# Optimization experiments

Measured on AMD Instinct MI355X. Metric: run time of the kernel, lower is better.

Reference implementation:

```python
import jax, jax.numpy as jnp
import numpy as np

N, TI, TO1 = 8, 200, 51
V, E, H, J, L = 1024, 512, 512, 512, 3
ENC_D = 512


def setup_inputs() -> dict:
    key = jax.random.key(0)
    ks = jax.random.split(key, 11)
    s = lambda k, shape, sc: jax.random.normal(k, shape, jnp.float32) * sc
    return {
        "enc_out": s(ks[0], (N, TI, ENC_D), 1.0),
        "tgt_pad": jax.random.randint(ks[1], (N, TO1), 0, V),
        "embed": s(ks[2], (V, E), 0.02),          # nn.Embedding weight
        "w_ih": s(ks[3], (L, 4 * H, E), 0.04),    # LSTM input-hidden (gate order i,f,g,o)
        "w_hh": s(ks[4], (L, 4 * H, H), 0.04),    # LSTM hidden-hidden
        "b_ih": s(ks[5], (L, 4 * H), 0.04),
        "b_hh": s(ks[6], (L, 4 * H), 0.04),
        "enc_w": s(ks[7], (J, ENC_D), 0.04),      # enc_proj (no bias)
        "dec_w": s(ks[8], (J, H), 0.04),          # dec_proj weight
        "dec_b": s(ks[9], (J,), 0.04),            # dec_proj bias
        "out_w": s(ks[10], (V, J), 0.04),         # output (no bias)
    }


def lstm_layer(x, wih, whh, bih, bhh):
    # x: [N, T, E] -> [N, T, H]; PyTorch LSTM gate order i, f, g, o
    n = x.shape[0]
    h0 = jnp.zeros((n, whh.shape[1]), x.dtype)
    c0 = jnp.zeros_like(h0)
    gin = jnp.einsum('nte,ge->ntg', x, wih) + bih + bhh  # precompute input contributions

    def step(carry, g_t):
        h, c = carry
        g = g_t + h @ whh.T
        i, f, gg, o = jnp.split(g, 4, axis=-1)
        c = jax.nn.sigmoid(f) * c + jax.nn.sigmoid(i) * jnp.tanh(gg)
        h = jax.nn.sigmoid(o) * jnp.tanh(c)
        return (h, c), h

    _, hs = jax.lax.scan(step, (h0, c0), jnp.swapaxes(gin, 0, 1))
    return jnp.swapaxes(hs, 0, 1)


def reference(enc_out, tgt_pad, embed, w_ih, w_hh, b_ih, b_hh, enc_w, dec_w, dec_b, out_w):
    # embedding lookup
    x = embed[tgt_pad]                                   # [N, To+1, E]
    # 3-layer unidirectional LSTM
    for l in range(w_ih.shape[0]):
        x = lstm_layer(x, w_ih[l], w_hh[l], b_ih[l], b_hh[l])
    # projections
    enc_p = jnp.einsum('ntd,jd->ntj', enc_out, enc_w)    # [N, Ti, J]
    dec_p = jnp.einsum('nud,jd->nuj', x, dec_w) + dec_b  # [N, To+1, J]
    # joint: broadcast add -> tanh -> output linear (no bias)
    add = enc_p[:, :, None, :] + dec_p[:, None, :, :]    # [N, Ti, To+1, J]
    return jnp.einsum('ntuj,vj->ntuv', jnp.tanh(add), out_w)  # [N, Ti, To+1, V]
```

## Files before the change

kernel.cpp:

```cpp
#include <hip/hip_runtime.h>
#include <cstdint>
#include <cstddef>

typedef __attribute__((ext_vector_type(4))) float f32x4;
typedef __attribute__((ext_vector_type(8))) short bf16x8;
typedef __attribute__((ext_vector_type(8))) unsigned short u16x8;
typedef __attribute__((ext_vector_type(4))) float float4v;
typedef __attribute__((ext_vector_type(2))) unsigned long long u64x2;
typedef unsigned long long ull;

#define NB   8
#define TIN  200
#define TO1  51
#define VSZ  1024
#define HSZ  512
static constexpr int MJOINT = NB * TIN * TO1;
static constexpr int MROWS  = TO1 * NB;

static constexpr size_t B_ENCBF = 0;
static constexpr size_t B_ENCW  = B_ENCBF + 1664ull*512*2;
static constexpr size_t B_DECW  = B_ENCW  + 512ull*512*2;
static constexpr size_t B_OUTW  = B_DECW  + 512ull*512*2;
static constexpr size_t B_WIH   = B_OUTW  + 1024ull*512*2;
static constexpr size_t B_WHH   = B_WIH   + 3ull*2048*512*2;
static constexpr size_t B_XTR   = B_WHH   + 3ull*2048*512*2;
static constexpr size_t B_BSUM  = B_XTR   + 4ull*408*512*2;
static constexpr size_t B_FLAGS = B_BSUM  + 3ull*2048*4;
static constexpr size_t B_ENCP  = B_FLAGS + 8192;
static constexpr size_t B_DECP  = B_ENCP  + 1664ull*512*4;
static constexpr size_t B_ABUF  = B_DECP  + 512ull*512*4;

__device__ __forceinline__ unsigned short f2bf(float f) {
  union { float f; unsigned u; } v; v.f = f;
  unsigned r = v.u + 0x7FFFu + ((v.u >> 16) & 1u);
  return (unsigned short)(r >> 16);
}
__device__ __forceinline__ float fast_tanh(float x) {
  float t = __expf(2.0f * x);
  return 1.0f - 2.0f / (t + 1.0f);
}
__device__ __forceinline__ float fast_sig(float x) {
  return 1.0f / (1.0f + __expf(-x));
}
__device__ __forceinline__ void gll16(const void* g, void* l) {
  __builtin_amdgcn_global_load_lds(
      (const __attribute__((address_space(1))) unsigned int*)g,
      (__attribute__((address_space(3))) unsigned int*)l, 16, 0, 0);
}
__device__ __forceinline__ void cvt8(const float* s, unsigned short* d) {
  const float4v* sp = (const float4v*)s;
  float4v x = sp[0], y = sp[1];
  u16x8 o;
  o[0]=f2bf(x[0]); o[1]=f2bf(x[1]); o[2]=f2bf(x[2]); o[3]=f2bf(x[3]);
  o[4]=f2bf(y[0]); o[5]=f2bf(y[1]); o[6]=f2bf(y[2]); o[7]=f2bf(y[3]);
  *(u16x8*)d = o;
}

static constexpr int N_ENC  = 102400;
static constexpr int N_ENCW = 32768;
static constexpr int N_DECW = 32768;
static constexpr int N_OUTW = 65536;
static constexpr int N_WIH  = 393216;
static constexpr int P0 = N_ENC, P1 = P0+N_ENCW, P2 = P1+N_DECW, P3 = P2+N_OUTW,
                     P4 = P3+N_WIH;

__global__ __launch_bounds__(256) void prep_all(const float* __restrict__ enc,
                                                const float* __restrict__ encw,
                                                const float* __restrict__ decw,
                                                const float* __restrict__ outw,
                                                const float* __restrict__ wih,
                                                const float* __restrict__ whh,
                                                const float* __restrict__ emb,
                                                const int* __restrict__ tgt,
                                                const float* __restrict__ bih,
                                                const float* __restrict__ bhh,
                                                unsigned short* __restrict__ d_enc,
                                                unsigned short* __restrict__ d_encw,
                                                unsigned short* __restrict__ d_decw,
                                                unsigned short* __restrict__ d_outw,
                                                unsigned short* __restrict__ d_wih,
                                                unsigned short* __restrict__ d_whh,
                                                unsigned short* __restrict__ x0,
                                                float* __restrict__ bsum,
                                                int* __restrict__ flags) {
  if (blockIdx.x == 0 && threadIdx.x < 96) flags[threadIdx.x * 16] = 0;
  if (blockIdx.x >= 4086) {
    int i = (blockIdx.x - 4086) * 2048 + threadIdx.x * 8;
#pragma unroll
    for (int k = 0; k < 8; ++k) bsum[i + k] = bih[i + k] + bhh[i + k];
    return;
  }
  if (blockIdx.x >= 3984) {
    int idx = (blockIdx.x - 3984) * 256 + threadIdx.x;
    if (idx >= MROWS * 64) return;
    int m = idx >> 6, kc = (idx & 63) * 8;
    int t = m >> 3, n = m & 7;
    int v = tgt[n * TO1 + t];
    cvt8(emb + (size_t)v * 512 + kc, x0 + (size_t)m * 512 + kc);
    return;
  }
  int i = blockIdx.x * 256 + threadIdx.x;
  const float* s; unsigned short* d; int rel;
  if      (i < P0) { s = enc;  d = d_enc;  rel = i; }
  else if (i < P1) { s = encw; d = d_encw; rel = i - P0; }
  else if (i < P2) { s = decw; d = d_decw; rel = i - P1; }
  else if (i < P3) { s = outw; d = d_outw; rel = i - P2; }
  else if (i < P4) { s = wih;  d = d_wih;  rel = i - P3; }
  else             { s = whh;  d = d_whh;  rel = i - P4; }
  cvt8(s + (size_t)rel * 8, d + (size_t)rel * 8);
}

__global__ __launch_bounds__(256) void gemm_bf16(const unsigned short* __restrict__ A,
                                                 const unsigned short* __restrict__ B,
                                                 float* __restrict__ C,
                                                 const float* __restrict__ bias,
                                                 int M, int N, int K) {
  __shared__ __align__(16) unsigned short lds[2][2][4096];
  const int tid = threadIdx.x;
  const int wave = tid >> 6, lane = tid & 63;
  const int lr = lane & 15, lg = lane >> 4;
  const int wm = (wave >> 1) * 64, wn = (wave & 1) * 64;
  const int xsl = (lg ^ (lr & 3)) << 3;

  const int nwg = gridDim.x * gridDim.y;
  const int id = blockIdx.y * gridDim.x + blockIdx.x;
  const int q = nwg >> 3, r = nwg & 7, xcd = id & 7, rest = id >> 3;
  const int nid = (xcd < r ? xcd * (q + 1) : r * (q + 1) + (xcd - r) * q) + rest;
  const size_t n0 = (size_t)(nid % gridDim.x) * 128;
  const size_t m0 = (size_t)(nid / gridDim.x) * 128;

  f32x4 acc[4][4];
#pragma unroll
  for (int i = 0; i < 4; ++i)
#pragma unroll
    for (int j = 0; j < 4; ++j) acc[i][j] = (f32x4){0.f, 0.f, 0.f, 0.f};

#define STAGE(bf, kt)                                                                 \
  do {                                                                                \
    _Pragma("unroll") for (int u = 0; u < 2; ++u) {                                   \
      const int s = u * 256 + tid;                                                    \
      const int row_ = s >> 2;                                                        \
      const int ch = (s & 3) ^ (row_ & 3);                                            \
      gll16(A + (m0 + row_) * (size_t)K + (kt) + ch * 8,                              \
            &lds[bf][0][(u * 256 + wave * 64) * 8]);                                  \
    }                                                                                 \
    _Pragma("unroll") for (int u = 0; u < 2; ++u) {                                   \
      const int s = u * 256 + tid;                                                    \
      const int row_ = s >> 2;                                                        \
      const int ch = (s & 3) ^ (row_ & 3);                                            \
      gll16(B + (n0 + row_) * (size_t)K + (kt) + ch * 8,                              \
            &lds[bf][1][(u * 256 + wave * 64) * 8]);                                  \
    }                                                                                 \
  } while (0)

  const int nt = K >> 5;
  int cur = 0;
  STAGE(0, 0);
  for (int t = 0; t < nt; ++t) {
    if (t + 1 < nt) {
      STAGE(cur ^ 1, (t + 1) * 32);
      asm volatile("s_waitcnt vmcnt(4)" ::: "memory");
    } else {
      asm volatile("s_waitcnt vmcnt(0)" ::: "memory");
    }
    __builtin_amdgcn_s_barrier();
    const unsigned short* As_ = lds[cur][0];
    const unsigned short* Bs_ = lds[cur][1];
    bf16x8 a[4], b[4];
#pragma unroll
    for (int i = 0; i < 4; ++i) a[i] = *(const bf16x8*)&As_[(wm + i * 16 + lr) * 32 + xsl];
#pragma unroll
    for (int j = 0; j < 4; ++j) b[j] = *(const bf16x8*)&Bs_[(wn + j * 16 + lr) * 32 + xsl];
    __builtin_amdgcn_s_setprio(1);
#pragma unroll
    for (int i = 0; i < 4; ++i)
#pragma unroll
      for (int j = 0; j < 4; ++j)
        acc[i][j] = __builtin_amdgcn_mfma_f32_16x16x32_bf16(a[i], b[j], acc[i][j], 0, 0, 0);
    __builtin_amdgcn_s_setprio(0);
    __builtin_amdgcn_s_barrier();
    cur ^= 1;
  }
#undef STAGE

  const int rq = lg * 4;
#pragma unroll
  for (int j = 0; j < 4; ++j) {
    const int col = (int)n0 + wn + j * 16 + lr;
    const float bv = bias ? bias[col] : 0.0f;
#pragma unroll
    for (int i = 0; i < 4; ++i) {
#pragma unroll
      for (int q2 = 0; q2 < 4; ++q2) {
        const long m = (long)m0 + wm + i * 16 + rq + q2;
        if (m < M) C[(size_t)m * N + col] = acc[i][j][q2] + bv;
      }
    }
  }
}

__global__ __launch_bounds__(512, 2) void gemm256(const unsigned short* __restrict__ A,
                                                  const unsigned short* __restrict__ B,
                                                  float* __restrict__ C,
                                                  int M, int N, int K) {
  __shared__ __align__(16) unsigned short lds[2][2][8192];
  const int tid = threadIdx.x;
  const int wave = tid >> 6, lane = tid & 63;
  const int lr = lane & 15, lg = lane >> 4;
  const int wr = (wave >> 2) * 128;
  const int wc = (wave & 3) * 64;

  const int nwg = gridDim.x * gridDim.y;
  const int id = blockIdx.y * gridDim.x + blockIdx.x;
  const int q = nwg >> 3, r = nwg & 7, xcd = id & 7, rest = id >> 3;
  const int nid = (xcd < r ? xcd * (q + 1) : r * (q + 1) + (xcd - r) * q) + rest;
  const size_t n0 = (size_t)(nid % gridDim.x) * 256;
  const size_t m0 = (size_t)(nid / gridDim.x) * 256;

  f32x4 acc[8][4];
#pragma unroll
  for (int i = 0; i < 8; ++i)
#pragma unroll
    for (int j = 0; j < 4; ++j) acc[i][j] = (f32x4){0.f, 0.f, 0.f, 0.f};

#define STG(bf, kt)                                                                    \
  do {                                                                                 \
    _Pragma("unroll") for (int u = 0; u < 2; ++u) {                                    \
      const int idx = u * 512 + tid;                                                   \
      const int row_ = idx >> 2;                                                       \
      const int ch = (idx & 3) ^ (row_ & 3);                                           \
      gll16(A + (m0 + row_) * (size_t)K + (kt) + ch * 8,                               \
            &lds[bf][0][(u * 512 + wave * 64) * 8]);                                   \
    }                                                                                  \
    _Pragma("unroll") for (int u = 0; u < 2; ++u) {                                    \
      const int idx = u * 512 + tid;                                                   \
      const int row_ = idx >> 2;                                                       \
      const int ch = (idx & 3) ^ (row_ & 3);                                           \
      gll16(B + (n0 + row_) * (size_t)K + (kt) + ch * 8,                               \
            &lds[bf][1][(u * 512 + wave * 64) * 8]);                                   \
    }                                                                                  \
  } while (0)

  const int nt = K >> 5;
  int cur = 0;
  STG(0, 0);
  for (int t = 0; t < nt; ++t) {
    if (t + 1 < nt) {
      STG(cur ^ 1, (t + 1) * 32);
      asm volatile("s_waitcnt vmcnt(4)" ::: "memory");
    } else {
      asm volatile("s_waitcnt vmcnt(0)" ::: "memory");
    }
    __builtin_amdgcn_s_barrier();
    const unsigned short* As_ = lds[cur][0];
    const unsigned short* Bs_ = lds[cur][1];
    bf16x8 b[4];
#pragma unroll
    for (int j = 0; j < 4; ++j) {
      const int rb = wc + j * 16 + lr;
      b[j] = *(const bf16x8*)&Bs_[rb * 32 + ((lg ^ (rb & 3)) << 3)];
    }
    __builtin_amdgcn_s_setprio(1);
#pragma unroll
    for (int i = 0; i < 8; ++i) {
      const int ra = wr + i * 16 + lr;
      bf16x8 a0 = *(const bf16x8*)&As_[ra * 32 + ((lg ^ (ra & 3)) << 3)];
#pragma unroll
      for (int j = 0; j < 4; ++j)
        acc[i][j] = __builtin_amdgcn_mfma_f32_16x16x32_bf16(a0, b[j], acc[i][j], 0, 0, 0);
    }
    __builtin_amdgcn_s_setprio(0);
    __builtin_amdgcn_s_barrier();
    cur ^= 1;
  }
#undef STG

#pragma unroll
  for (int i = 0; i < 8; ++i) {
#pragma unroll
    for (int q2 = 0; q2 < 4; ++q2) {
      const long m = (long)m0 + wr + i * 16 + lg * 4 + q2;
      if (m < M) {
        float* crow = C + (size_t)m * N + n0 + wc;
#pragma unroll
        for (int j = 0; j < 4; ++j) crow[j * 16 + lr] = acc[i][j][q2];
      }
    }
  }
}

__global__ __launch_bounds__(256) void tanha_kernel(const float* __restrict__ encp,
                                                    const float* __restrict__ decp,
                                                    unsigned short* __restrict__ Ab) {
  size_t idx = (size_t)blockIdx.x * 256 + threadIdx.x;
  int m = (int)(idx >> 6);
  int kc = ((int)idx & 63) * 8;
  if (m >= 81664) return;
  u16x8 o;
  if (m >= MJOINT) {
    o[0]=0;o[1]=0;o[2]=0;o[3]=0;o[4]=0;o[5]=0;o[6]=0;o[7]=0;
  } else {
    int n = m / (TIN * TO1);
    int rem = m - n * (TIN * TO1);
    int t = rem / TO1;
    int u = rem - t * TO1;
    const float4v* ep = (const float4v*)(encp + ((size_t)n * TIN + t) * 512 + kc);
    const float4v* dp = (const float4v*)(decp + ((size_t)u * 8 + n) * 512 + kc);
    float4v e0 = ep[0], e1 = ep[1], d0 = dp[0], d1 = dp[1];
    o[0]=f2bf(fast_tanh(e0[0]+d0[0])); o[1]=f2bf(fast_tanh(e0[1]+d0[1]));
    o[2]=f2bf(fast_tanh(e0[2]+d0[2])); o[3]=f2bf(fast_tanh(e0[3]+d0[3]));
    o[4]=f2bf(fast_tanh(e1[0]+d1[0])); o[5]=f2bf(fast_tanh(e1[1]+d1[1]));
    o[6]=f2bf(fast_tanh(e1[2]+d1[2])); o[7]=f2bf(fast_tanh(e1[3]+d1[3]));
  }
  *(u16x8*)(Ab + (size_t)m * 512 + kc) = o;
}

__global__ __launch_bounds__(256) void rnn_enc_kernel(const unsigned short* __restrict__ wih,
                                                      const unsigned short* __restrict__ whh,
                                                      const float* __restrict__ bsum,
                                                      unsigned short* __restrict__ xtr,
                                                      int* __restrict__ flags,
                                                      const unsigned short* __restrict__ eA,
                                                      const unsigned short* __restrict__ eB,
                                                      float* __restrict__ eC) {
  __shared__ __align__(16) unsigned short w_s[64 * 1024];
  __shared__ __align__(16) unsigned short x_s[8 * 512];
  __shared__ __align__(16) unsigned short h_s[8 * 512];
  __shared__ float gates_s[4][8][16];

  const int tid = threadIdx.x;
  const int wave = tid >> 6, lane = tid & 63;
  const int lr = lane & 15, lg = lane >> 4;

  if (blockIdx.x >= 96) {
    unsigned short* eld = w_s;
    const int g = blockIdx.x - 96;
    const int wm = (wave >> 1) * 64, wn = (wave & 1) * 64;
    const int xsl = (lg ^ (lr & 3)) << 3;
    const int nwg = 52;
    const int q = nwg >> 3, r = nwg & 7, xcd = g & 7, rest = g >> 3;
    const int nid = (xcd < r ? xcd * (q + 1) : r * (q + 1) + (xcd - r) * q) + rest;
    const size_t n0 = (size_t)(nid & 3) * 128;
    const size_t m0 = (size_t)(nid >> 2) * 128;

    f32x4 acc[4][4];
#pragma unroll
    for (int i = 0; i < 4; ++i)
#pragma unroll
      for (int j = 0; j < 4; ++j) acc[i][j] = (f32x4){0.f, 0.f, 0.f, 0.f};

#define ESTG(bf, kt)                                                                   \
    do {                                                                               \
      _Pragma("unroll") for (int u = 0; u < 2; ++u) {                                  \
        const int s = u * 256 + tid;                                                   \
        const int row_ = s >> 2;                                                       \
        const int ch = (s & 3) ^ (row_ & 3);                                           \
        gll16(eA + (m0 + row_) * 512 + (kt) + ch * 8,                                  \
              &eld[(bf) * 8192 + (u * 256 + wave * 64) * 8]);                          \
      }                                                                                \
      _Pragma("unroll") for (int u = 0; u < 2; ++u) {                                  \
        const int s = u * 256 + tid;                                                   \
        const int row_ = s >> 2;                                                       \
        const int ch = (s & 3) ^ (row_ & 3);                                           \
        gll16(eB + (n0 + row_) * 512 + (kt) + ch * 8,                                  \
              &eld[(bf) * 8192 + 4096 + (u * 256 + wave * 64) * 8]);                   \
      }                                                                                \
    } while (0)

    int cur = 0;
    ESTG(0, 0);
    for (int t = 0; t < 16; ++t) {
      if (t + 1 < 16) {
        ESTG(cur ^ 1, (t + 1) * 32);
        asm volatile("s_waitcnt vmcnt(4)" ::: "memory");
      } else {
        asm volatile("s_waitcnt vmcnt(0)" ::: "memory");
      }
      __builtin_amdgcn_s_barrier();
      const unsigned short* As_ = eld + cur * 8192;
      const unsigned short* Bs_ = As_ + 4096;
      bf16x8 a[4], b[4];
#pragma unroll
      for (int i = 0; i < 4; ++i) a[i] = *(const bf16x8*)&As_[(wm + i * 16 + lr) * 32 + xsl];
#pragma unroll
      for (int j = 0; j < 4; ++j) b[j] = *(const bf16x8*)&Bs_[(wn + j * 16 + lr) * 32 + xsl];
      __builtin_amdgcn_s_setprio(1);
#pragma unroll
      for (int i = 0; i < 4; ++i)
#pragma unroll
        for (int j = 0; j < 4; ++j)
          acc[i][j] = __builtin_amdgcn_mfma_f32_16x16x32_bf16(a[i], b[j], acc[i][j], 0, 0, 0);
      __builtin_amdgcn_s_setprio(0);
      __builtin_amdgcn_s_barrier();
      cur ^= 1;
    }
#undef ESTG

    const int rq = lg * 4;
#pragma unroll
    for (int j = 0; j < 4; ++j) {
      const int col = (int)n0 + wn + j * 16 + lr;
#pragma unroll
      for (int i = 0; i < 4; ++i) {
#pragma unroll
        for (int q2 = 0; q2 < 4; ++q2) {
          const long m = (long)m0 + wm + i * 16 + rq + q2;
          eC[(size_t)m * 512 + col] = acc[i][j][q2];
        }
      }
    }
    return;
  }

  const int l = blockIdx.x >> 5;
  const int b32 = blockIdx.x & 31;
  const int hid0 = b32 << 4;
  const int r7 = lr & 7;
  const int rw = wave * 16 + lr;

  {
    const int rl = tid >> 2;
    const int qt = tid & 3;
    const size_t R = (size_t)l * 2048 + (size_t)(rl >> 4) * 512 + hid0 + (rl & 15);
    const unsigned short* s0 = wih + R * 512;
    const unsigned short* s1 = whh + R * 512;
#pragma unroll
    for (int i = 0; i < 32; ++i) {
      int c = qt * 32 + i;
      bf16x8 wv = (c < 64) ? *(const bf16x8*)&s0[c * 8] : *(const bf16x8*)&s1[(c - 64) * 8];
      *(bf16x8*)&w_s[rl * 1024 + ((c ^ (rl & 7)) << 3)] = wv;
    }
  }
  const float bias = bsum[(size_t)l * 2048 + (size_t)wave * 512 + hid0 + lr];

  const unsigned short* xin = xtr + (size_t)l * MROWS * 512;
  unsigned short* xout = xtr + (size_t)(l + 1) * MROWS * 512;
  float c_reg = 0.f;
  const int srow = tid >> 5;
  const int sc = tid & 31;
  __syncthreads();

#define ALOAD(P) __hip_atomic_load((P), __ATOMIC_RELAXED, __HIP_MEMORY_SCOPE_AGENT)

  f32x4 ax0, ax1;

  if (l > 0) {
    if (wave == 0) {
      for (;;) {
        bool ok_ = true;
        if (lane < 32)
          ok_ = ALOAD(&flags[((l - 1) * 32 + lane) * 16]) >= 1;
        if (__all(ok_)) break;
        __builtin_amdgcn_s_sleep(1);
      }
    }
  }
  __syncthreads();
  {
    const ull* px = (const ull*)(xin + (size_t)srow * 512);
#pragma unroll
    for (int k_ = 0; k_ < 2; ++k_) {
      const int c_ = sc + k_ * 32;
      ull v0 = ALOAD(px + c_ * 2), v1 = ALOAD(px + c_ * 2 + 1);
      *(u64x2*)&x_s[srow * 512 + ((c_ ^ srow) << 3)] = (u64x2){v0, v1};
    }
  }
  __syncthreads();
  ax0 = (f32x4){0.f, 0.f, 0.f, 0.f};
  ax1 = (f32x4){0.f, 0.f, 0.f, 0.f};
#pragma unroll
  for (int c16 = 0; c16 < 16; ++c16) {
    const int cc = c16 * 4 + lg;
    bf16x8 av = *(const bf16x8*)&x_s[r7 * 512 + ((cc ^ r7) << 3)];
    bf16x8 bv = *(const bf16x8*)&w_s[rw * 1024 + ((cc ^ r7) << 3)];
    if (c16 & 1) ax1 = __builtin_amdgcn_mfma_f32_16x16x32_bf16(av, bv, ax1, 0, 0, 0);
    else         ax0 = __builtin_amdgcn_mfma_f32_16x16x32_bf16(av, bv, ax0, 0, 0, 0);
  }

  for (int t = 0; t < TO1; ++t) {
    const bool doH = (t > 0);
    const bool doX = (t + 1 < TO1);
    if (doH || (doX && l > 0)) {
      if (wave == 0) {
        for (;;) {
          bool ok_ = true;
          if (lane < 32) {
            if (doH) ok_ = ALOAD(&flags[(l * 32 + lane) * 16]) >= t;
          } else {
            if (doX && l > 0)
              ok_ = ALOAD(&flags[((l - 1) * 32 + (lane - 32)) * 16]) >= t + 2;
          }
          if (__all(ok_)) break;
          __builtin_amdgcn_s_sleep(1);
        }
      }
    }
    __syncthreads();

    {
      ull vh[4], vx[4];
      const ull* ph = (const ull*)(xout + ((size_t)(t - 1) * 8 + srow) * 512);
      const ull* px = (const ull*)(xin + ((size_t)(t + 1) * 8 + srow) * 512);
#pragma unroll
      for (int k_ = 0; k_ < 2; ++k_) {
        const int c_ = sc + k_ * 32;
        if (doH) { vh[2 * k_] = ALOAD(ph + c_ * 2); vh[2 * k_ + 1] = ALOAD(ph + c_ * 2 + 1); }
        if (doX) { vx[2 * k_] = ALOAD(px + c_ * 2); vx[2 * k_ + 1] = ALOAD(px + c_ * 2 + 1); }
      }
#pragma unroll
      for (int k_ = 0; k_ < 2; ++k_) {
        const int c_ = sc + k_ * 32;
        if (doH) *(u64x2*)&h_s[srow * 512 + ((c_ ^ srow) << 3)] = (u64x2){vh[2 * k_], vh[2 * k_ + 1]};
        if (doX) *(u64x2*)&x_s[srow * 512 + ((c_ ^ srow) << 3)] = (u64x2){vx[2 * k_], vx[2 * k_ + 1]};
      }
    }
    __syncthreads();

    f32x4 acc0 = ax0, acc1 = ax1;
    if (doH) {
#pragma unroll
      for (int c16 = 0; c16 < 16; ++c16) {
        const int cc = c16 * 4 + lg;
        bf16x8 av = *(const bf16x8*)&h_s[r7 * 512 + ((cc ^ r7) << 3)];
        bf16x8 bv = *(const bf16x8*)&w_s[rw * 1024 + (((64 + cc) ^ r7) << 3)];
        if (c16 & 1) acc1 = __builtin_amdgcn_mfma_f32_16x16x32_bf16(av, bv, acc1, 0, 0, 0);
        else         acc0 = __builtin_amdgcn_mfma_f32_16x16x32_bf16(av, bv, acc0, 0, 0, 0);
      }
    }

    {
      f32x4 g = acc0 + acc1;
      const int nb4 = lg * 4;
#pragma unroll
      for (int q2 = 0; q2 < 4; ++q2) {
        int n = nb4 + q2;
        if (n < 8) gates_s[wave][n][lr] = g[q2] + bias;
      }
    }
    __syncthreads();
    if (tid < 128) {
      const int n = tid >> 4, j = tid & 15;
      float gi = gates_s[0][n][j], gf = gates_s[1][n][j];
      float gg = gates_s[2][n][j], go = gates_s[3][n][j];
      c_reg = fast_sig(gf) * c_reg + fast_sig(gi) * fast_tanh(gg);
      float ht = fast_sig(go) * fast_tanh(c_reg);
      float htn = __shfl_down(ht, 1);
      if (!(j & 1)) {
        unsigned pk = (unsigned)f2bf(ht) | ((unsigned)f2bf(htn) << 16);
        unsigned* dst = (unsigned*)(xout + ((size_t)t * 8 + n) * 512 + hid0 + j);
        __hip_atomic_store(dst, pk, __ATOMIC_RELAXED, __HIP_MEMORY_SCOPE_AGENT);
      }
    }
    asm volatile("s_waitcnt vmcnt(0)" ::: "memory");
    __syncthreads();
    if (tid == 0)
      __hip_atomic_store(&flags[(l * 32 + b32) * 16], t + 1,
                         __ATOMIC_RELAXED, __HIP_MEMORY_SCOPE_AGENT);

    if (doX) {
      ax0 = (f32x4){0.f, 0.f, 0.f, 0.f};
      ax1 = (f32x4){0.f, 0.f, 0.f, 0.f};
#pragma unroll
      for (int c16 = 0; c16 < 16; ++c16) {
        const int cc = c16 * 4 + lg;
        bf16x8 av = *(const bf16x8*)&x_s[r7 * 512 + ((cc ^ r7) << 3)];
        bf16x8 bv = *(const bf16x8*)&w_s[rw * 1024 + ((cc ^ r7) << 3)];
        if (c16 & 1) ax1 = __builtin_amdgcn_mfma_f32_16x16x32_bf16(av, bv, ax1, 0, 0, 0);
        else         ax0 = __builtin_amdgcn_mfma_f32_16x16x32_bf16(av, bv, ax0, 0, 0, 0);
      }
    }
  }
#undef ALOAD
}

extern "C" void kernel_launch(void* const* d_in, const int* in_sizes, int n_in,
                              void* d_out, int out_size, void* d_ws, size_t ws_size,
                              hipStream_t stream) {
  (void)in_sizes; (void)n_in; (void)out_size; (void)ws_size;
  const float* enc_out = (const float*)d_in[0];
  const int*   tgt     = (const int*)d_in[1];
  const float* embed   = (const float*)d_in[2];
  const float* w_ih    = (const float*)d_in[3];
  const float* w_hh    = (const float*)d_in[4];
  const float* b_ih    = (const float*)d_in[5];
  const float* b_hh    = (const float*)d_in[6];
  const float* enc_w   = (const float*)d_in[7];
  const float* dec_w   = (const float*)d_in[8];
  const float* dec_b   = (const float*)d_in[9];
  const float* out_w   = (const float*)d_in[10];

  char* ws = (char*)d_ws;
  unsigned short* enc_bf  = (unsigned short*)(ws + B_ENCBF);
  unsigned short* encw_bf = (unsigned short*)(ws + B_ENCW);
  unsigned short* decw_bf = (unsigned short*)(ws + B_DECW);
  unsigned short* outw_bf = (unsigned short*)(ws + B_OUTW);
  unsigned short* wih_bf  = (unsigned short*)(ws + B_WIH);
  unsigned short* whh_bf  = (unsigned short*)(ws + B_WHH);
  unsigned short* xtr     = (unsigned short*)(ws + B_XTR);
  float* bsum  = (float*)(ws + B_BSUM);
  int*   flags = (int*)(ws + B_FLAGS);
  float* encp  = (float*)(ws + B_ENCP);
  float* decp  = (float*)(ws + B_DECP);
  unsigned short* abuf = (unsigned short*)(ws + B_ABUF);
  float* Cout  = (float*)d_out;

  prep_all<<<4089, 256, 0, stream>>>(enc_out, enc_w, dec_w, out_w, w_ih, w_hh,
                                     embed, tgt, b_ih, b_hh,
                                     enc_bf, encw_bf, decw_bf, outw_bf, wih_bf, whh_bf,
                                     xtr, bsum, flags);

  rnn_enc_kernel<<<148, 256, 0, stream>>>(wih_bf, whh_bf, bsum, xtr, flags,
                                          enc_bf, encw_bf, encp);

  gemm_bf16<<<dim3(4, 4), 256, 0, stream>>>(xtr + 3ull * MROWS * 512, decw_bf, decp, dec_b,
                                            MROWS, 512, 512);
  tanha_kernel<<<20416, 256, 0, stream>>>(encp, decp, abuf);
  gemm256<<<dim3(4, 319), 512, 0, stream>>>(abuf, outw_bf, Cout, MJOINT, VSZ, 512);
}
```

Measured before the change: 347.7 us.

## Fuse decoder projection and tanh-join into persistent RNN kernel with flag-driven workers

Removes the separate dec_proj GEMM and tanh/add kernels. 102 extra workgroups are added to the persistent RNN/encoder kernel. Each one polls the layer-3 timestep flags and a new encoder-projection completion counter, then computes its dec_p row with MFMA and writes the tanh(enc_p+dec_p) bf16 activations. The aim is to hide joint-input preparation behind the serial LSTM recurrence and save two launches. The risks are that the bandwidth-heavy tanh stage now runs on only 102 workgroups, the last timestep's work stays exposed at the tail, all workgroups must be co-resident, and the padding rows of abuf are no longer zeroed.

New measurement: 336.4 us. -3.2%, faster.

```diff
diff --git a/kernel.cpp b/kernel.cpp
--- a/kernel.cpp
+++ b/kernel.cpp
@@ -55,6 +55,8 @@
   o[4]=f2bf(y[0]); o[5]=f2bf(y[1]); o[6]=f2bf(y[2]); o[7]=f2bf(y[3]);
   *(u16x8*)d = o;
 }
+#define ALOAD(P)     __hip_atomic_load((P), __ATOMIC_RELAXED, __HIP_MEMORY_SCOPE_AGENT)
+#define ASTORE(P, V) __hip_atomic_store((P), (V), __ATOMIC_RELAXED, __HIP_MEMORY_SCOPE_AGENT)
 
 static constexpr int N_ENC  = 102400;
 static constexpr int N_ENCW = 32768;
@@ -83,7 +85,7 @@
                                                 unsigned short* __restrict__ x0,
                                                 float* __restrict__ bsum,
                                                 int* __restrict__ flags) {
-  if (blockIdx.x == 0 && threadIdx.x < 96) flags[threadIdx.x * 16] = 0;
+  if (blockIdx.x == 0 && threadIdx.x < 97) flags[threadIdx.x * 16] = 0;
   if (blockIdx.x >= 4086) {
     int i = (blockIdx.x - 4086) * 2048 + threadIdx.x * 8;
 #pragma unroll
@@ -108,95 +110,6 @@
   else if (i < P4) { s = wih;  d = d_wih;  rel = i - P3; }
   else             { s = whh;  d = d_whh;  rel = i - P4; }
   cvt8(s + (size_t)rel * 8, d + (size_t)rel * 8);
-}
-
-__global__ __launch_bounds__(256) void gemm_bf16(const unsigned short* __restrict__ A,
-                                                 const unsigned short* __restrict__ B,
-                                                 float* __restrict__ C,
-                                                 const float* __restrict__ bias,
-                                                 int M, int N, int K) {
-  __shared__ __align__(16) unsigned short lds[2][2][4096];
-  const int tid = threadIdx.x;
-  const int wave = tid >> 6, lane = tid & 63;
-  const int lr = lane & 15, lg = lane >> 4;
-  const int wm = (wave >> 1) * 64, wn = (wave & 1) * 64;
-  const int xsl = (lg ^ (lr & 3)) << 3;
-
-  const int nwg = gridDim.x * gridDim.y;
-  const int id = blockIdx.y * gridDim.x + blockIdx.x;
-  const int q = nwg >> 3, r = nwg & 7, xcd = id & 7, rest = id >> 3;
-  const int nid = (xcd < r ? xcd * (q + 1) : r * (q + 1) + (xcd - r) * q) + rest;
-  const size_t n0 = (size_t)(nid % gridDim.x) * 128;
-  const size_t m0 = (size_t)(nid / gridDim.x) * 128;
-
-  f32x4 acc[4][4];
-#pragma unroll
-  for (int i = 0; i < 4; ++i)
-#pragma unroll
-    for (int j = 0; j < 4; ++j) acc[i][j] = (f32x4){0.f, 0.f, 0.f, 0.f};
-
-#define STAGE(bf, kt)                                                                 \
-  do {                                                                                \
-    _Pragma("unroll") for (int u = 0; u < 2; ++u) {                                   \
-      const int s = u * 256 + tid;                                                    \
-      const int row_ = s >> 2;                                                        \
-      const int ch = (s & 3) ^ (row_ & 3);                                            \
-      gll16(A + (m0 + row_) * (size_t)K + (kt) + ch * 8,                              \
-            &lds[bf][0][(u * 256 + wave * 64) * 8]);                                  \
-    }                                                                                 \
-    _Pragma("unroll") for (int u = 0; u < 2; ++u) {                                   \
-      const int s = u * 256 + tid;                                                    \
-      const int row_ = s >> 2;                                                        \
-      const int ch = (s & 3) ^ (row_ & 3);                                            \
-      gll16(B + (n0 + row_) * (size_t)K + (kt) + ch * 8,                              \
-            &lds[bf][1][(u * 256 + wave * 64) * 8]);                                  \
-    }                                                                                 \
-  } while (0)
-
-  const int nt = K >> 5;
-  int cur = 0;
-  STAGE(0, 0);
-  for (int t = 0; t < nt; ++t) {
-    if (t + 1 < nt) {
-      STAGE(cur ^ 1, (t + 1) * 32);
-      asm volatile("s_waitcnt vmcnt(4)" ::: "memory");
-    } else {
-      asm volatile("s_waitcnt vmcnt(0)" ::: "memory");
-    }
-    __builtin_amdgcn_s_barrier();
-    const unsigned short* As_ = lds[cur][0];
-    const unsigned short* Bs_ = lds[cur][1];
-    bf16x8 a[4], b[4];
-#pragma unroll
-    for (int i = 0; i < 4; ++i) a[i] = *(const bf16x8*)&As_[(wm + i * 16 + lr) * 32 + xsl];
-#pragma unroll
-    for (int j = 0; j < 4; ++j) b[j] = *(const bf16x8*)&Bs_[(wn + j * 16 + lr) * 32 + xsl];
-    __builtin_amdgcn_s_setprio(1);
-#pragma unroll
-    for (int i = 0; i < 4; ++i)
-#pragma unroll
-      for (int j = 0; j < 4; ++j)
-        acc[i][j] = __builtin_amdgcn_mfma_f32_16x16x32_bf16(a[i], b[j], acc[i][j], 0, 0, 0);
-    __builtin_amdgcn_s_setprio(0);
-    __builtin_amdgcn_s_barrier();
-    cur ^= 1;
-  }
-#undef STAGE
-
-  const int rq = lg * 4;
-#pragma unroll
-  for (int j = 0; j < 4; ++j) {
-    const int col = (int)n0 + wn + j * 16 + lr;
-    const float bv = bias ? bias[col] : 0.0f;
-#pragma unroll
-    for (int i = 0; i < 4; ++i) {
-#pragma unroll
-      for (int q2 = 0; q2 < 4; ++q2) {
-        const long m = (long)m0 + wm + i * 16 + rq + q2;
-        if (m < M) C[(size_t)m * N + col] = acc[i][j][q2] + bv;
-      }
-    }
-  }
 }
 
 __global__ __launch_bounds__(512, 2) void gemm256(const unsigned short* __restrict__ A,
@@ -289,40 +202,18 @@
   }
 }
 
-__global__ __launch_bounds__(256) void tanha_kernel(const float* __restrict__ encp,
-                                                    const float* __restrict__ decp,
-                                                    unsigned short* __restrict__ Ab) {
-  size_t idx = (size_t)blockIdx.x * 256 + threadIdx.x;
-  int m = (int)(idx >> 6);
-  int kc = ((int)idx & 63) * 8;
-  if (m >= 81664) return;
-  u16x8 o;
-  if (m >= MJOINT) {
-    o[0]=0;o[1]=0;o[2]=0;o[3]=0;o[4]=0;o[5]=0;o[6]=0;o[7]=0;
-  } else {
-    int n = m / (TIN * TO1);
-    int rem = m - n * (TIN * TO1);
-    int t = rem / TO1;
-    int u = rem - t * TO1;
-    const float4v* ep = (const float4v*)(encp + ((size_t)n * TIN + t) * 512 + kc);
-    const float4v* dp = (const float4v*)(decp + ((size_t)u * 8 + n) * 512 + kc);
-    float4v e0 = ep[0], e1 = ep[1], d0 = dp[0], d1 = dp[1];
-    o[0]=f2bf(fast_tanh(e0[0]+d0[0])); o[1]=f2bf(fast_tanh(e0[1]+d0[1]));
-    o[2]=f2bf(fast_tanh(e0[2]+d0[2])); o[3]=f2bf(fast_tanh(e0[3]+d0[3]));
-    o[4]=f2bf(fast_tanh(e1[0]+d1[0])); o[5]=f2bf(fast_tanh(e1[1]+d1[1]));
-    o[6]=f2bf(fast_tanh(e1[2]+d1[2])); o[7]=f2bf(fast_tanh(e1[3]+d1[3]));
-  }
-  *(u16x8*)(Ab + (size_t)m * 512 + kc) = o;
-}
-
-__global__ __launch_bounds__(256) void rnn_enc_kernel(const unsigned short* __restrict__ wih,
-                                                      const unsigned short* __restrict__ whh,
-                                                      const float* __restrict__ bsum,
-                                                      unsigned short* __restrict__ xtr,
-                                                      int* __restrict__ flags,
-                                                      const unsigned short* __restrict__ eA,
-                                                      const unsigned short* __restrict__ eB,
-                                                      float* __restrict__ eC) {
+__global__ __launch_bounds__(256) void mega_kernel(const unsigned short* __restrict__ wih,
+                                                   const unsigned short* __restrict__ whh,
+                                                   const float* __restrict__ bsum,
+                                                   unsigned short* __restrict__ xtr,
+                                                   int* __restrict__ flags,
+                                                   const unsigned short* __restrict__ eA,
+                                                   const unsigned short* __restrict__ eB,
+                                                   float* __restrict__ eC,
+                                                   const unsigned short* __restrict__ decw,
+                                                   const float* __restrict__ dec_b,
+                                                   const float* __restrict__ encp,
+                                                   unsigned short* __restrict__ abuf) {
   __shared__ __align__(16) unsigned short w_s[64 * 1024];
   __shared__ __align__(16) unsigned short x_s[8 * 512];
   __shared__ __align__(16) unsigned short h_s[8 * 512];
@@ -331,6 +222,81 @@
   const int tid = threadIdx.x;
   const int wave = tid >> 6, lane = tid & 63;
   const int lr = lane & 15, lg = lane >> 4;
+  const int r7 = lr & 7;
+
+  if (blockIdx.x >= 148) {
+    const int wkr = blockIdx.x - 148;
+    unsigned short* h3_s = x_s;
+    float* decp_row = (float*)w_s;
+    const unsigned short* xtr3 = xtr + 3ull * MROWS * 512;
+#pragma unroll 1
+    for (int k = 0; k < 4; ++k) {
+      const int j = wkr + 102 * k;
+      const int u = j >> 3;
+      const int p = j & 7;
+      if (wave == 0) {
+        for (;;) {
+          bool ok = true;
+          if (lane < 32) ok = ALOAD(&flags[(64 + lane) * 16]) >= u + 1;
+          else if (lane == 32) ok = ALOAD(&flags[96 * 16]) >= 52;
+          if (__all(ok)) break;
+          __builtin_amdgcn_s_sleep(1);
+        }
+      }
+      __syncthreads();
+      {
+        const int sr2 = tid >> 5, sc2 = tid & 31;
+        const ull* ph = (const ull*)(xtr3 + ((size_t)u * 8 + sr2) * 512);
+#pragma unroll
+        for (int k2 = 0; k2 < 2; ++k2) {
+          const int c_ = sc2 + k2 * 32;
+          ull v0 = ALOAD(ph + c_ * 2), v1 = ALOAD(ph + c_ * 2 + 1);
+          *(u64x2*)&h3_s[sr2 * 512 + ((c_ ^ sr2) << 3)] = (u64x2){v0, v1};
+        }
+      }
+      __syncthreads();
+      {
+        const int colbase = wave * 128;
+#pragma unroll
+        for (int ct = 0; ct < 8; ++ct) {
+          f32x4 acc = (f32x4){0.f, 0.f, 0.f, 0.f};
+          const int col = colbase + ct * 16 + lr;
+#pragma unroll
+          for (int c16 = 0; c16 < 16; ++c16) {
+            const int cc = c16 * 4 + lg;
+            bf16x8 av = *(const bf16x8*)&h3_s[r7 * 512 + ((cc ^ r7) << 3)];
+            bf16x8 bv = *(const bf16x8*)&decw[(size_t)col * 512 + cc * 8];
+            acc = __builtin_amdgcn_mfma_f32_16x16x32_bf16(av, bv, acc, 0, 0, 0);
+          }
+#pragma unroll
+          for (int q2 = 0; q2 < 4; ++q2)
+            if (lg * 4 + q2 == p) decp_row[col] = acc[q2] + dec_b[col];
+        }
+      }
+      __syncthreads();
+      {
+        const int tr = tid >> 6;
+        const int colc = (lane) * 8;
+        for (int pass = 0; pass < 50; ++pass) {
+          const int nt = p * 200 + pass * 4 + tr;
+          const ull* pe = (const ull*)(encp + (size_t)nt * 512 + colc);
+          ull ev[4];
+#pragma unroll
+          for (int k2 = 0; k2 < 4; ++k2) ev[k2] = ALOAD(pe + k2);
+          float ef[8];
+          *(u64x2*)&ef[0] = (u64x2){ev[0], ev[1]};
+          *(u64x2*)&ef[4] = (u64x2){ev[2], ev[3]};
+          u16x8 o;
+#pragma unroll
+          for (int w2 = 0; w2 < 8; ++w2)
+            o[w2] = f2bf(fast_tanh(ef[w2] + decp_row[colc + w2]));
+          *(u16x8*)&abuf[((size_t)nt * TO1 + u) * 512 + colc] = o;
+        }
+      }
+      __syncthreads();
+    }
+    return;
+  }
 
   if (blockIdx.x >= 96) {
     unsigned short* eld = w_s;
@@ -405,17 +371,20 @@
 #pragma unroll
         for (int q2 = 0; q2 < 4; ++q2) {
           const long m = (long)m0 + wm + i * 16 + rq + q2;
-          eC[(size_t)m * 512 + col] = acc[i][j][q2];
+          ASTORE(&eC[(size_t)m * 512 + col], acc[i][j][q2]);
         }
       }
     }
+    asm volatile("s_waitcnt vmcnt(0)" ::: "memory");
+    __syncthreads();
+    if (tid == 0)
+      __hip_atomic_fetch_add(&flags[96 * 16], 1, __ATOMIC_RELAXED, __HIP_MEMORY_SCOPE_AGENT);
     return;
   }
 
   const int l = blockIdx.x >> 5;
   const int b32 = blockIdx.x & 31;
   const int hid0 = b32 << 4;
-  const int r7 = lr & 7;
   const int rw = wave * 16 + lr;
 
   {
@@ -439,8 +408,6 @@
   const int srow = tid >> 5;
   const int sc = tid & 31;
   __syncthreads();
-
-#define ALOAD(P) __hip_atomic_load((P), __ATOMIC_RELAXED, __HIP_MEMORY_SCOPE_AGENT)
 
   f32x4 ax0, ax1;
 
@@ -547,15 +514,13 @@
       float htn = __shfl_down(ht, 1);
       if (!(j & 1)) {
         unsigned pk = (unsigned)f2bf(ht) | ((unsigned)f2bf(htn) << 16);
-        unsigned* dst = (unsigned*)(xout + ((size_t)t * 8 + n) * 512 + hid0 + j);
-        __hip_atomic_store(dst, pk, __ATOMIC_RELAXED, __HIP_MEMORY_SCOPE_AGENT);
+        ASTORE((unsigned*)(xout + ((size_t)t * 8 + n) * 512 + hid0 + j), pk);
       }
     }
     asm volatile("s_waitcnt vmcnt(0)" ::: "memory");
     __syncthreads();
     if (tid == 0)
-      __hip_atomic_store(&flags[(l * 32 + b32) * 16], t + 1,
-                         __ATOMIC_RELAXED, __HIP_MEMORY_SCOPE_AGENT);
+      ASTORE(&flags[(l * 32 + b32) * 16], t + 1);
 
     if (doX) {
       ax0 = (f32x4){0.f, 0.f, 0.f, 0.f};
@@ -570,7 +535,6 @@
       }
     }
   }
-#undef ALOAD
 }
 
 extern "C" void kernel_launch(void* const* d_in, const int* in_sizes, int n_in,
@@ -600,7 +564,6 @@
   float* bsum  = (float*)(ws + B_BSUM);
   int*   flags = (int*)(ws + B_FLAGS);
   float* encp  = (float*)(ws + B_ENCP);
-  float* decp  = (float*)(ws + B_DECP);
   unsigned short* abuf = (unsigned short*)(ws + B_ABUF);
   float* Cout  = (float*)d_out;
 
@@ -609,11 +572,9 @@
                                      enc_bf, encw_bf, decw_bf, outw_bf, wih_bf, whh_bf,
                                      xtr, bsum, flags);
 
-  rnn_enc_kernel<<<148, 256, 0, stream>>>(wih_bf, whh_bf, bsum, xtr, flags,
-                                          enc_bf, encw_bf, encp);
-
-  gemm_bf16<<<dim3(4, 4), 256, 0, stream>>>(xtr + 3ull * MROWS * 512, decw_bf, decp, dec_b,
-                                            MROWS, 512, 512);
-  tanha_kernel<<<20416, 256, 0, stream>>>(encp, decp, abuf);
+  mega_kernel<<<250, 256, 0, stream>>>(wih_bf, whh_bf, bsum, xtr, flags,
+                                       enc_bf, encw_bf, encp,
+                                       decw_bf, dec_b, encp, abuf);
+
   gemm256<<<dim3(4, 319), 512, 0, stream>>>(abuf, outw_bf, Cout, MJOINT, VSZ, 512);
 }
```
